# Kernel optimization log

Measured on AMD Instinct MI355X. Metric: run time of the kernel, lower is better.

## Reference

```python
import jax, jax.numpy as jnp
import numpy as np

# fatigue class -> emotion target distribution; row 3 is the uniform fallback
_TABLE = np.array([
    [0.05, 0.02, 0.03, 0.4, 0.05, 0.4, 0.05],
    [0.05, 0.05, 0.05, 0.05, 0.3, 0.05, 0.45],
    [0.1, 0.15, 0.2, 0.02, 0.35, 0.03, 0.15],
    [1.0 / 7.0] * 7,
], dtype=np.float32)

B = 4_000_000

def setup_inputs() -> dict:
    key = jax.random.key(0)
    k1, k2, k3 = jax.random.split(key, 3)
    fatigue_logits = jax.random.normal(k1, (B, 3), dtype=jnp.float32)
    emotion_logits = jax.random.normal(k2, (B, 7), dtype=jnp.float32)
    fatigue_targets = jax.random.randint(k3, (B,), 0, 4, dtype=jnp.int64)
    return {"fatigue_logits": fatigue_logits,
            "emotion_logits": emotion_logits,
            "fatigue_targets": fatigue_targets}

def reference(fatigue_logits, emotion_logits, fatigue_targets):
    eps = 1e-8
    table = jnp.asarray(_TABLE)
    # targets outside {0,1,2} map to the uniform row (index 3)
    idx = jnp.where((fatigue_targets >= 0) & (fatigue_targets <= 2), fatigue_targets, 3)
    target = table[idx]                      # [B, 7] gather from tiny LUT
    target = target + eps
    target = target / jnp.sum(target, axis=-1, keepdims=True)
    probs = jax.nn.softmax(emotion_logits, axis=-1)
    log_input = jnp.log(probs + eps)
    # F.kl_div(log_input, target, reduction='batchmean')
    kl = jnp.sum(target * (jnp.log(target) - log_input)) / target.shape[0]
    return kl
```

## Files before the change

### kernel.cpp

```cpp
#include <hip/hip_runtime.h>
#include <cmath>

struct KLC {
    float w0[7], w1[7], w2[7], w3[7];
    float cst0, cst1, cst2, cst3;
};

__device__ __forceinline__ float row_kl7(
    float x0, float x1, float x2, float x3, float x4, float x5, float x6,
    int t, const KLC& kc)
{
    int c = ((unsigned)t <= 2u) ? t : 3;

    float m = fmaxf(fmaxf(fmaxf(x0, x1), fmaxf(x2, x3)),
                    fmaxf(fmaxf(x4, x5), x6));

    float Z = __expf(x0 - m) + __expf(x1 - m) + __expf(x2 - m) + __expf(x3 - m)
            + __expf(x4 - m) + __expf(x5 - m) + __expf(x6 - m);

    float d0 = fmaf(kc.w0[6], x6, fmaf(kc.w0[5], x5, fmaf(kc.w0[4], x4,
               fmaf(kc.w0[3], x3, fmaf(kc.w0[2], x2, fmaf(kc.w0[1], x1, kc.w0[0] * x0))))));
    float d1 = fmaf(kc.w1[6], x6, fmaf(kc.w1[5], x5, fmaf(kc.w1[4], x4,
               fmaf(kc.w1[3], x3, fmaf(kc.w1[2], x2, fmaf(kc.w1[1], x1, kc.w1[0] * x0))))));
    float d2 = fmaf(kc.w2[6], x6, fmaf(kc.w2[5], x5, fmaf(kc.w2[4], x4,
               fmaf(kc.w2[3], x3, fmaf(kc.w2[2], x2, fmaf(kc.w2[1], x1, kc.w2[0] * x0))))));
    float d3 = fmaf(kc.w3[6], x6, fmaf(kc.w3[5], x5, fmaf(kc.w3[4], x4,
               fmaf(kc.w3[3], x3, fmaf(kc.w3[2], x2, fmaf(kc.w3[1], x1, kc.w3[0] * x0))))));

    float dw = (c == 0) ? d0 : (c == 1) ? d1 : (c == 2) ? d2 : d3;
    float cs = (c == 0) ? kc.cst0 : (c == 1) ? kc.cst1 : (c == 2) ? kc.cst2 : kc.cst3;

    return cs - dw + m + __logf(Z);
}

__global__ __launch_bounds__(256) void kl_main(
    const float* __restrict__ logits,
    const int*   __restrict__ tgt,
    int nchunks,
    double* __restrict__ partial,
    KLC kc)
{
    __shared__ float4 lds4[1792];
    const float4* __restrict__ lg4 = (const float4*)logits;
    const int4*   __restrict__ tg4 = (const int4*)tgt;

    const int t = threadIdx.x;
    float local = 0.0f;

    for (int ch = blockIdx.x; ch < nchunks; ch += gridDim.x) {
        const long long base4 = (long long)ch * 1792;

        float4 r0 = lg4[base4 + 0 * 256 + t];
        float4 r1 = lg4[base4 + 1 * 256 + t];
        float4 r2 = lg4[base4 + 2 * 256 + t];
        float4 r3 = lg4[base4 + 3 * 256 + t];
        float4 r4 = lg4[base4 + 4 * 256 + t];
        float4 r5 = lg4[base4 + 5 * 256 + t];
        float4 r6 = lg4[base4 + 6 * 256 + t];
        int4   tq = tg4[(long long)ch * 256 + t];

        __syncthreads();
        lds4[0 * 256 + t] = r0;
        lds4[1 * 256 + t] = r1;
        lds4[2 * 256 + t] = r2;
        lds4[3 * 256 + t] = r3;
        lds4[4 * 256 + t] = r4;
        lds4[5 * 256 + t] = r5;
        lds4[6 * 256 + t] = r6;
        __syncthreads();

        float4 c0 = lds4[t * 7 + 0];
        float4 c1 = lds4[t * 7 + 1];
        float4 c2 = lds4[t * 7 + 2];
        float4 c3 = lds4[t * 7 + 3];
        float4 c4 = lds4[t * 7 + 4];
        float4 c5 = lds4[t * 7 + 5];
        float4 c6 = lds4[t * 7 + 6];

        local += row_kl7(c0.x, c0.y, c0.z, c0.w, c1.x, c1.y, c1.z, tq.x, kc);
        local += row_kl7(c1.w, c2.x, c2.y, c2.z, c2.w, c3.x, c3.y, tq.y, kc);
        local += row_kl7(c3.z, c3.w, c4.x, c4.y, c4.z, c4.w, c5.x, tq.z, kc);
        local += row_kl7(c5.y, c5.z, c5.w, c6.x, c6.y, c6.z, c6.w, tq.w, kc);
    }

    #pragma unroll
    for (int off = 32; off > 0; off >>= 1)
        local += __shfl_down(local, off, 64);

    __shared__ float smem[4];
    int lane = threadIdx.x & 63;
    int wid  = threadIdx.x >> 6;
    if (lane == 0) smem[wid] = local;
    __syncthreads();
    if (threadIdx.x == 0)
        partial[blockIdx.x] = (double)(smem[0] + smem[1] + smem[2] + smem[3]);
}

__global__ __launch_bounds__(256) void kl_reduce(
    const float* __restrict__ logits,
    const int*   __restrict__ tgt,
    long long tail_start, int tail,
    const double* __restrict__ partial, int nb,
    float* __restrict__ out, int B, KLC kc)
{
    double s = 0.0;
    for (int i = threadIdx.x; i < nb; i += 256) s += partial[i];

    float tl = 0.0f;
    for (int r = threadIdx.x; r < tail; r += 256) {
        const float* x = logits + (tail_start + r) * 7;
        tl += row_kl7(x[0], x[1], x[2], x[3], x[4], x[5], x[6],
                      tgt[tail_start + r], kc);
    }
    s += (double)tl;

    #pragma unroll
    for (int off = 32; off > 0; off >>= 1)
        s += __shfl_down(s, off, 64);

    __shared__ double smem[4];
    int lane = threadIdx.x & 63;
    int wid  = threadIdx.x >> 6;
    if (lane == 0) smem[wid] = s;
    __syncthreads();
    if (threadIdx.x == 0)
        out[0] = (float)((smem[0] + smem[1] + smem[2] + smem[3]) / (double)B);
}

extern "C" void kernel_launch(void* const* d_in, const int* in_sizes, int n_in,
                              void* d_out, int out_size, void* d_ws, size_t ws_size,
                              hipStream_t stream) {
    const float* emotion = (const float*)d_in[1];
    const int*   targets = (const int*)d_in[2];
    float*  out     = (float*)d_out;
    double* partial = (double*)d_ws;

    const int B = in_sizes[2];
    const int nchunks = B / 1024;
    const int tail = B - nchunks * 1024;
    const long long tail_start = (long long)nchunks * 1024;

    int nb = 1024;
    if (nb > nchunks && nchunks > 0) nb = nchunks;
    if ((size_t)nb * sizeof(double) > ws_size)
        nb = (int)(ws_size / sizeof(double));

    static const double T[4][7] = {
        {0.05, 0.02, 0.03, 0.4, 0.05, 0.4, 0.05},
        {0.05, 0.05, 0.05, 0.05, 0.3, 0.05, 0.45},
        {0.1, 0.15, 0.2, 0.02, 0.35, 0.03, 0.15},
        {1.0/7.0, 1.0/7.0, 1.0/7.0, 1.0/7.0, 1.0/7.0, 1.0/7.0, 1.0/7.0},
    };
    const double eps = 1e-8;
    KLC kc;
    float* wrows[4] = { kc.w0, kc.w1, kc.w2, kc.w3 };
    float* csts[4]  = { &kc.cst0, &kc.cst1, &kc.cst2, &kc.cst3 };
    for (int c = 0; c < 4; ++c) {
        double s = 0.0;
        for (int j = 0; j < 7; ++j) s += T[c][j] + eps;
        double cst = 0.0;
        for (int j = 0; j < 7; ++j) {
            double w = (T[c][j] + eps) / s;
            wrows[c][j] = (float)w;
            cst += w * std::log(w);
        }
        *csts[c] = (float)cst;
    }

    kl_main<<<nb, 256, 0, stream>>>(emotion, targets, nchunks, partial, kc);
    kl_reduce<<<1, 256, 0, stream>>>(emotion, targets, tail_start, tail,
                                     partial, nb, out, B, kc);
}
```

Before: 200.0 us.

## Drop max-subtraction, batch logs over row quads, load rows directly without LDS

Removes the per-row max stabilisation and evaluates one log over the product of four rows' partition sums instead of one log per row. Drops the LDS transpose and grid-stride loop: each thread now loads 8 contiguous rows with nontemporal vector loads, and one block is launched per 2048 rows. This cuts ALU, transcendental and sync work in a memory-bound kernel. The costs are possible overflow or underflow for large logits, uncoalesced strided per-thread loads, and a grid of about 2000 blocks, each writing a partial that the single reduce block must sum. If ws_size forces nb lower, rows in the extra blocks are silently dropped.

After: 224.6 us. +12.3%, slower.

```diff
diff --git a/kernel.cpp b/kernel.cpp
--- a/kernel.cpp
+++ b/kernel.cpp
@@ -6,17 +6,17 @@
     float cst0, cst1, cst2, cst3;
 };
 
-__device__ __forceinline__ float row_kl7(
+typedef __attribute__((ext_vector_type(4))) float f4;
+typedef __attribute__((ext_vector_type(4))) int   i4;
+
+__device__ __forceinline__ void row_part(
     float x0, float x1, float x2, float x3, float x4, float x5, float x6,
-    int t, const KLC& kc)
+    int t, const KLC& kc, float& lin, float& Z)
 {
     int c = ((unsigned)t <= 2u) ? t : 3;
 
-    float m = fmaxf(fmaxf(fmaxf(x0, x1), fmaxf(x2, x3)),
-                    fmaxf(fmaxf(x4, x5), x6));
-
-    float Z = __expf(x0 - m) + __expf(x1 - m) + __expf(x2 - m) + __expf(x3 - m)
-            + __expf(x4 - m) + __expf(x5 - m) + __expf(x6 - m);
+    Z = __expf(x0) + __expf(x1) + __expf(x2) + __expf(x3)
+      + __expf(x4) + __expf(x5) + __expf(x6);
 
     float d0 = fmaf(kc.w0[6], x6, fmaf(kc.w0[5], x5, fmaf(kc.w0[4], x4,
                fmaf(kc.w0[3], x3, fmaf(kc.w0[2], x2, fmaf(kc.w0[1], x1, kc.w0[0] * x0))))));
@@ -29,58 +29,53 @@
 
     float dw = (c == 0) ? d0 : (c == 1) ? d1 : (c == 2) ? d2 : d3;
     float cs = (c == 0) ? kc.cst0 : (c == 1) ? kc.cst1 : (c == 2) ? kc.cst2 : kc.cst3;
+    lin = cs - dw;
+}
 
-    return cs - dw + m + __logf(Z);
+__device__ __forceinline__ float quad_kl(
+    f4 c0, f4 c1, f4 c2, f4 c3, f4 c4, f4 c5, f4 c6, i4 tq, const KLC& kc)
+{
+    float l0, l1, l2, l3, Z0, Z1, Z2, Z3;
+    row_part(c0.x, c0.y, c0.z, c0.w, c1.x, c1.y, c1.z, tq.x, kc, l0, Z0);
+    row_part(c1.w, c2.x, c2.y, c2.z, c2.w, c3.x, c3.y, tq.y, kc, l1, Z1);
+    row_part(c3.z, c3.w, c4.x, c4.y, c4.z, c4.w, c5.x, tq.z, kc, l2, Z2);
+    row_part(c5.y, c5.z, c5.w, c6.x, c6.y, c6.z, c6.w, tq.w, kc, l3, Z3);
+    return l0 + l1 + l2 + l3 + __logf((Z0 * Z1) * (Z2 * Z3));
 }
 
 __global__ __launch_bounds__(256) void kl_main(
     const float* __restrict__ logits,
     const int*   __restrict__ tgt,
-    int nchunks,
+    int noct,
     double* __restrict__ partial,
     KLC kc)
 {
-    __shared__ float4 lds4[1792];
-    const float4* __restrict__ lg4 = (const float4*)logits;
-    const int4*   __restrict__ tg4 = (const int4*)tgt;
+    const f4* __restrict__ lg = (const f4*)logits;
+    const i4* __restrict__ tg = (const i4*)tgt;
 
-    const int t = threadIdx.x;
+    int tid = blockIdx.x * blockDim.x + threadIdx.x;
     float local = 0.0f;
+    if (tid < noct) {
+        long long b = (long long)tid * 14;
+        f4 a0 = __builtin_nontemporal_load(&lg[b + 0]);
+        f4 a1 = __builtin_nontemporal_load(&lg[b + 1]);
+        f4 a2 = __builtin_nontemporal_load(&lg[b + 2]);
+        f4 a3 = __builtin_nontemporal_load(&lg[b + 3]);
+        f4 a4 = __builtin_nontemporal_load(&lg[b + 4]);
+        f4 a5 = __builtin_nontemporal_load(&lg[b + 5]);
+        f4 a6 = __builtin_nontemporal_load(&lg[b + 6]);
+        f4 b0 = __builtin_nontemporal_load(&lg[b + 7]);
+        f4 b1 = __builtin_nontemporal_load(&lg[b + 8]);
+        f4 b2 = __builtin_nontemporal_load(&lg[b + 9]);
+        f4 b3 = __builtin_nontemporal_load(&lg[b + 10]);
+        f4 b4 = __builtin_nontemporal_load(&lg[b + 11]);
+        f4 b5 = __builtin_nontemporal_load(&lg[b + 12]);
+        f4 b6 = __builtin_nontemporal_load(&lg[b + 13]);
+        i4 t0 = __builtin_nontemporal_load(&tg[(long long)tid * 2 + 0]);
+        i4 t1 = __builtin_nontemporal_load(&tg[(long long)tid * 2 + 1]);
 
-    for (int ch = blockIdx.x; ch < nchunks; ch += gridDim.x) {
-        const long long base4 = (long long)ch * 1792;
-
-        float4 r0 = lg4[base4 + 0 * 256 + t];
-        float4 r1 = lg4[base4 + 1 * 256 + t];
-        float4 r2 = lg4[base4 + 2 * 256 + t];
-        float4 r3 = lg4[base4 + 3 * 256 + t];
-        float4 r4 = lg4[base4 + 4 * 256 + t];
-        float4 r5 = lg4[base4 + 5 * 256 + t];
-        float4 r6 = lg4[base4 + 6 * 256 + t];
-        int4   tq = tg4[(long long)ch * 256 + t];
-
-        __syncthreads();
-        lds4[0 * 256 + t] = r0;
-        lds4[1 * 256 + t] = r1;
-        lds4[2 * 256 + t] = r2;
-        lds4[3 * 256 + t] = r3;
-        lds4[4 * 256 + t] = r4;
-        lds4[5 * 256 + t] = r5;
-        lds4[6 * 256 + t] = r6;
-        __syncthreads();
-
-        float4 c0 = lds4[t * 7 + 0];
-        float4 c1 = lds4[t * 7 + 1];
-        float4 c2 = lds4[t * 7 + 2];
-        float4 c3 = lds4[t * 7 + 3];
-        float4 c4 = lds4[t * 7 + 4];
-        float4 c5 = lds4[t * 7 + 5];
-        float4 c6 = lds4[t * 7 + 6];
-
-        local += row_kl7(c0.x, c0.y, c0.z, c0.w, c1.x, c1.y, c1.z, tq.x, kc);
-        local += row_kl7(c1.w, c2.x, c2.y, c2.z, c2.w, c3.x, c3.y, tq.y, kc);
-        local += row_kl7(c3.z, c3.w, c4.x, c4.y, c4.z, c4.w, c5.x, tq.z, kc);
-        local += row_kl7(c5.y, c5.z, c5.w, c6.x, c6.y, c6.z, c6.w, tq.w, kc);
+        local  = quad_kl(a0, a1, a2, a3, a4, a5, a6, t0, kc);
+        local += quad_kl(b0, b1, b2, b3, b4, b5, b6, t1, kc);
     }
 
     #pragma unroll
@@ -109,8 +104,10 @@
     float tl = 0.0f;
     for (int r = threadIdx.x; r < tail; r += 256) {
         const float* x = logits + (tail_start + r) * 7;
-        tl += row_kl7(x[0], x[1], x[2], x[3], x[4], x[5], x[6],
-                      tgt[tail_start + r], kc);
+        float lin, Z;
+        row_part(x[0], x[1], x[2], x[3], x[4], x[5], x[6],
+                 tgt[tail_start + r], kc, lin, Z);
+        tl += lin + __logf(Z);
     }
     s += (double)tl;
 
@@ -136,12 +133,11 @@
     double* partial = (double*)d_ws;
 
     const int B = in_sizes[2];
-    const int nchunks = B / 1024;
-    const int tail = B - nchunks * 1024;
-    const long long tail_start = (long long)nchunks * 1024;
+    const int noct = B / 8;
+    const int tail = B - noct * 8;
+    const long long tail_start = (long long)noct * 8;
 
-    int nb = 1024;
-    if (nb > nchunks && nchunks > 0) nb = nchunks;
+    int nb = (noct + 255) / 256;
     if ((size_t)nb * sizeof(double) > ws_size)
         nb = (int)(ws_size / sizeof(double));
 
@@ -167,7 +163,7 @@
         *csts[c] = (float)cst;
     }
 
-    kl_main<<<nb, 256, 0, stream>>>(emotion, targets, nchunks, partial, kc);
+    kl_main<<<nb, 256, 0, stream>>>(emotion, targets, noct, partial, kc);
     kl_reduce<<<1, 256, 0, stream>>>(emotion, targets, tail_start, tail,
                                      partial, nb, out, B, kc);
 }
```
